# Performance work log

Hardware: AMD Instinct MI355X
Metric: run time of the kernel (lower is better)

The kernel has to match this reference:

```python
import jax, jax.numpy as jnp
import numpy as np
import math

FACTOR = 5


def _prob_attention(queries, keys, values, index_sample):
    # queries/keys/values: [B, H, L, D]; index_sample: [L_Q, sample_k] int
    B, H, L_Q, D = queries.shape
    L_K = keys.shape[2]
    u = min(FACTOR * int(math.ceil(math.log(L_Q))), L_Q)  # n_top queries

    # --- _prob_QK: random-sampled scores, heuristic M, top-u query selection ---
    # gather sampled keys per query position: [B, H, L_Q, sample_k, D]
    K_sample = keys[:, :, index_sample, :]
    Q_K_sample = jnp.einsum('bhqd,bhqkd->bhqk', queries, K_sample)  # [B,H,L_Q,sample_k]
    M = Q_K_sample.max(axis=-1) - Q_K_sample.sum(axis=-1) / L_K      # [B,H,L_Q]
    M_top = jax.lax.top_k(M, u)[1]                                   # [B,H,u] indices

    # gather the selected queries and compute full scores against all keys
    Q_reduce = jnp.take_along_axis(queries, M_top[..., None], axis=2)  # [B,H,u,D]
    scores = jnp.einsum('bhud,bhkd->bhuk', Q_reduce, keys)             # [B,H,u,L_K]

    # scale: original does `scale = self.scale or 1/sqrt(D)`; with scale=True this
    # multiplies by True (i.e. *1), so scores are left unscaled -- faithful.

    # --- causal ProbMask: triu(1) rows gathered at the selected query indices ---
    causal = jnp.triu(jnp.ones((L_Q, L_K), dtype=bool), 1)  # [L_Q, L_K]
    row_mask = causal[M_top]                                 # [B,H,u,L_K]
    scores = jnp.where(row_mask, -jnp.inf, scores)

    attn = jax.nn.softmax(scores, axis=-1)                   # [B,H,u,L_K]

    # --- initial context (mask_flag=True): cumulative sum of V over time ---
    context = jnp.cumsum(values, axis=2)                     # [B,H,L_Q,D]

    # --- scatter-update context at selected query positions ---
    upd = jnp.einsum('bhuk,bhkd->bhud', attn, values)        # [B,H,u,D]
    b_idx = jnp.arange(B)[:, None, None]
    h_idx = jnp.arange(H)[None, :, None]
    context = context.at[b_idx, h_idx, M_top].set(upd)

    return jnp.transpose(context, (0, 2, 1, 3))              # [B,L_Q,H,D]


def setup_inputs() -> dict:
    key = jax.random.key(0)
    kq, kk, kv, ki = jax.random.split(key, 4)
    B, H, L, D = 4, 8, 2048, 64
    sample_k = FACTOR * int(math.ceil(math.log(L)))  # 40
    queries = jax.random.normal(kq, (B, H, L, D), dtype=jnp.float32)
    keys = jax.random.normal(kk, (B, H, L, D), dtype=jnp.float32)
    values = jax.random.normal(kv, (B, H, L, D), dtype=jnp.float32)
    index_sample = jax.random.randint(ki, (L, sample_k), 0, L)
    return {"queries": queries, "keys": keys, "values": values,
            "index_sample": index_sample}


def reference(queries, keys, values, index_sample):
    return _prob_attention(queries, keys, values, index_sample)
```

## Files before the change

kernel.cpp:

```cpp
#include <hip/hip_runtime.h>
#include <math.h>

#define B_ 4
#define H_ 8
#define L_ 2048
#define D_ 64
#define SK_ 40
#define U_ 40
#define CK 256
#define NCHUNK (L_ / CK)
#define QG 8
#define NQG (U_ / QG)
#define CSB 32
#define SEG2 16
#define NSEG2 (L_ / SEG2)
#define PB 256

__global__ __launch_bounds__(1024) void k_mcs(
    const float* __restrict__ Q, const float* __restrict__ K,
    const int* __restrict__ idxs, const float* __restrict__ V,
    float* __restrict__ M, float* __restrict__ pfx) {
  if (blockIdx.x < CSB) {
    __shared__ float wt[16][64];
    int bh = blockIdx.x;
    int w = threadIdx.x >> 6, lane = threadIdx.x & 63;
    const float* Vb = V + (size_t)bh * L_ * D_;
    float pres[8];
    float pre = 0.f;
#pragma unroll
    for (int i = 0; i < 8; ++i) {
      int base = w * 128 + i * SEG2;
      float s = 0.f;
      for (int l = 0; l < SEG2; ++l) s += Vb[(size_t)(base + l) * D_ + lane];
      pres[i] = pre;
      pre += s;
    }
    wt[w][lane] = pre;
    __syncthreads();
    float base = 0.f;
    for (int ww = 0; ww < 16; ++ww) {
      float v = wt[ww][lane];
      if (ww < w) base += v;
    }
#pragma unroll
    for (int i = 0; i < 8; ++i)
      pfx[((size_t)bh * NSEG2 + w * 8 + i) * D_ + lane] = base + pres[i];
    return;
  }

  int blk = blockIdx.x - CSB;
  int x = blk & 7;
  int j = blk >> 3;
  int bh = ((j >> 7) << 3) | x;
  int qc = j & 127;
  int wave = threadIdx.x >> 6;
  int lane = threadIdx.x & 63;
  int q = qc * 16 + wave;

  int g  = lane >> 3;
  int li = lane & 7;

  const float4* qrow = (const float4*)(Q + ((size_t)bh * L_ + q) * D_);
  float4 qa = qrow[li], qb = qrow[li + 8];
  int myidx = (lane < SK_) ? idxs[q * SK_ + lane] : 0;
  const float* Kb = K + (size_t)bh * L_ * D_;

  int kis[5];
#pragma unroll
  for (int t = 0; t < 5; ++t) kis[t] = __shfl(myidx, t * 8 + g, 64);

  float4 ka[5], kb[5];
#pragma unroll
  for (int t = 0; t < 5; ++t) {
    const float4* kr = (const float4*)(Kb + (size_t)kis[t] * D_);
    ka[t] = kr[li];
    kb[t] = kr[li + 8];
  }

  float d[5];
#pragma unroll
  for (int t = 0; t < 5; ++t) {
    d[t] = qa.x * ka[t].x + qa.y * ka[t].y + qa.z * ka[t].z + qa.w * ka[t].w
         + qb.x * kb[t].x + qb.y * kb[t].y + qb.z * kb[t].z + qb.w * kb[t].w;
  }
  float mx = -INFINITY, sm = 0.f;
#pragma unroll
  for (int t = 0; t < 5; ++t) {
    float v = d[t];
    v += __shfl_xor(v, 1, 64);
    v += __shfl_xor(v, 2, 64);
    v += __shfl_xor(v, 4, 64);
    mx = fmaxf(mx, v);
    sm += v;
  }
  mx = fmaxf(mx, __shfl_xor(mx, 8, 64));
  mx = fmaxf(mx, __shfl_xor(mx, 16, 64));
  mx = fmaxf(mx, __shfl_xor(mx, 32, 64));
  sm += __shfl_xor(sm, 8, 64);
  sm += __shfl_xor(sm, 16, 64);
  sm += __shfl_xor(sm, 32, 64);
  if (lane == 0) M[bh * L_ + q] = mx - sm * (1.0f / (float)L_);
}

__global__ __launch_bounds__(1024) void k_topk(
    const float* __restrict__ M, const float* __restrict__ V,
    const float* __restrict__ pfx, int* __restrict__ Mtop,
    float* __restrict__ out) {
  if (blockIdx.x >= CSB) {
    int bid = blockIdx.x - CSB;
    int bh = bid >> 3, oct = bid & 7;
    int b = bh >> 3, h = bh & 7;
    int w = threadIdx.x >> 6, lane = threadIdx.x & 63;
    int seg = oct * 16 + w;
    float run = pfx[((size_t)bh * NSEG2 + seg) * D_ + lane];
    const float* Vb = V + (size_t)bh * L_ * D_;
    int base = seg * SEG2;
    for (int l = 0; l < SEG2; ++l) {
      int gl = base + l;
      run += Vb[(size_t)gl * D_ + lane];
      out[(((size_t)b * L_ + gl) * H_ + h) * D_ + lane] = run;
    }
    return;
  }

  __shared__ unsigned keys[L_];
  __shared__ int hist[256];
  __shared__ int Gs[256];
  __shared__ unsigned ctl_prefix;
  __shared__ int ctl_need, ctl_cnt, ctl_min;
  __shared__ int wmin[16];
  int bh = blockIdx.x;
  int tid = threadIdx.x;

  for (int i = tid; i < L_; i += 1024) {
    unsigned u = __float_as_uint(M[bh * L_ + i]);
    keys[i] = (u & 0x80000000u) ? ~u : (u | 0x80000000u);
  }
  if (tid == 0) { ctl_prefix = 0u; ctl_need = U_; ctl_cnt = 0; }
  __syncthreads();

  unsigned prefix = 0u, pmask = 0u;
#pragma unroll
  for (int pass = 0; pass < 4; ++pass) {
    int shift = 24 - 8 * pass;
    if (tid < 256) hist[tid] = 0;
    __syncthreads();
    for (int i = tid; i < L_; i += 1024) {
      unsigned k = keys[i];
      if ((k & pmask) == prefix) atomicAdd(&hist[(k >> shift) & 0xffu], 1);
    }
    __syncthreads();
    if (tid < 64) {
      int b0 = tid * 4;
      int h0 = hist[b0], h1 = hist[b0 + 1], h2 = hist[b0 + 2], h3 = hist[b0 + 3];
      int gs = h0 + h1 + h2 + h3;
      int S = gs;
#pragma unroll
      for (int d = 1; d < 64; d <<= 1) {
        int v = __shfl_down(S, d, 64);
        if (tid + d < 64) S += v;
      }
      int E = S - gs;
      Gs[b0 + 3] = E;
      Gs[b0 + 2] = E + h3;
      Gs[b0 + 1] = E + h3 + h2;
      Gs[b0 + 0] = E + h3 + h2 + h1;
    }
    __syncthreads();
    int need = ctl_need;
    if (tid < 256) {
      int G = Gs[tid], h = hist[tid];
      if (G < need && need <= G + h) {
        ctl_prefix = prefix | ((unsigned)tid << shift);
        ctl_need = need - G;
      }
    }
    __syncthreads();
    prefix = ctl_prefix;
    pmask |= (0xffu << shift);
  }

  unsigned v40 = prefix;
  int tiesNeeded = ctl_need;
  __syncthreads();

  for (int i = tid; i < L_; i += 1024) {
    if (keys[i] > v40) {
      int slot = atomicAdd(&ctl_cnt, 1);
      Mtop[bh * U_ + slot] = i;
    }
  }
  __syncthreads();
  int base = ctl_cnt;
  int last = -1;
  for (int t = 0; t < tiesNeeded; ++t) {
    int lmin = 0x7fffffff;
    for (int i = tid; i < L_; i += 1024)
      if (keys[i] == v40 && i > last) lmin = min(lmin, i);
#pragma unroll
    for (int d = 32; d > 0; d >>= 1) lmin = min(lmin, __shfl_xor(lmin, d, 64));
    if ((tid & 63) == 0) wmin[tid >> 6] = lmin;
    __syncthreads();
    if (tid == 0) {
      int m = wmin[0];
      for (int w = 1; w < 16; ++w) m = min(m, wmin[w]);
      Mtop[bh * U_ + base + t] = m;
      ctl_min = m;
    }
    __syncthreads();
    last = ctl_min;
  }
}

__global__ __launch_bounds__(256) void k_attn_part(
    const float* __restrict__ Q, const float* __restrict__ K,
    const float* __restrict__ V, const int* __restrict__ Mtop,
    float* __restrict__ pm, float* __restrict__ ps, float* __restrict__ pacc) {
  int blk = blockIdx.x;
  int x = blk & 7;
  int j = blk >> 3;
  int bh = (j / 40) * 8 + x;
  int rem = j % 40;
  int c  = rem / NQG;
  int qg = rem % NQG;

  int tid = threadIdx.x;
  int w = tid >> 6, lane = tid & 63;
  __shared__ float Qs[QG][D_];
  __shared__ float P[QG][CK];
  __shared__ float pvred[4][QG][D_];
  __shared__ int q0s[QG];
  if (tid < QG) q0s[tid] = Mtop[bh * U_ + qg * QG + tid];
  __syncthreads();
  for (int i = tid; i < QG * D_; i += 256) {
    int u = i >> 6, d = i & 63;
    Qs[u][d] = Q[((size_t)bh * L_ + q0s[u]) * D_ + d];
  }
  __syncthreads();

  int kg = c * CK + tid;
  const float4* kr = (const float4*)(K + ((size_t)bh * L_ + kg) * D_);
  float4 kv[16];
#pragma unroll
  for (int j4 = 0; j4 < 16; ++j4) kv[j4] = kr[j4];
#pragma unroll
  for (int u = 0; u < QG; ++u) {
    float acc = 0.f;
#pragma unroll
    for (int j4 = 0; j4 < 16; ++j4) {
      float4 qv = *(const float4*)&Qs[u][j4 * 4];
      acc += qv.x * kv[j4].x + qv.y * kv[j4].y + qv.z * kv[j4].z + qv.w * kv[j4].w;
    }
    P[u][tid] = (kg <= q0s[u]) ? acc : -INFINITY;
  }
  __syncthreads();

#pragma unroll
  for (int uu = 0; uu < 2; ++uu) {
    int u = w * 2 + uu;
    float v0 = P[u][lane], v1 = P[u][lane + 64];
    float v2 = P[u][lane + 128], v3 = P[u][lane + 192];
    float m = fmaxf(fmaxf(v0, v1), fmaxf(v2, v3));
    for (int o = 32; o > 0; o >>= 1) m = fmaxf(m, __shfl_xor(m, o, 64));
    float e0 = (v0 == -INFINITY) ? 0.f : expf(v0 - m);
    float e1 = (v1 == -INFINITY) ? 0.f : expf(v1 - m);
    float e2 = (v2 == -INFINITY) ? 0.f : expf(v2 - m);
    float e3 = (v3 == -INFINITY) ? 0.f : expf(v3 - m);
    float s = e0 + e1 + e2 + e3;
    for (int o = 32; o > 0; o >>= 1) s += __shfl_xor(s, o, 64);
    P[u][lane] = e0; P[u][lane + 64] = e1;
    P[u][lane + 128] = e2; P[u][lane + 192] = e3;
    if (lane == 0) {
      int p = (bh * NCHUNK + c) * U_ + qg * QG + u;
      pm[p] = m; ps[p] = s;
    }
  }
  __syncthreads();

  const float* Vb = V + ((size_t)bh * L_ + c * CK + w * 64) * D_;
  float acc[QG];
#pragma unroll
  for (int u = 0; u < QG; ++u) acc[u] = 0.f;
  for (int k4 = 0; k4 < 16; ++k4) {
    float4 pv[QG];
#pragma unroll
    for (int u = 0; u < QG; ++u) pv[u] = *(const float4*)&P[u][w * 64 + k4 * 4];
    float va = Vb[(size_t)(k4 * 4 + 0) * D_ + lane];
    float vb = Vb[(size_t)(k4 * 4 + 1) * D_ + lane];
    float vc = Vb[(size_t)(k4 * 4 + 2) * D_ + lane];
    float vd = Vb[(size_t)(k4 * 4 + 3) * D_ + lane];
#pragma unroll
    for (int u = 0; u < QG; ++u)
      acc[u] += pv[u].x * va + pv[u].y * vb + pv[u].z * vc + pv[u].w * vd;
  }
#pragma unroll
  for (int u = 0; u < QG; ++u) pvred[w][u][lane] = acc[u];
  __syncthreads();
#pragma unroll
  for (int uu = 0; uu < 2; ++uu) {
    int u = w * 2 + uu;
    float tot = pvred[0][u][lane] + pvred[1][u][lane] +
                pvred[2][u][lane] + pvred[3][u][lane];
    int p = (bh * NCHUNK + c) * U_ + qg * QG + u;
    pacc[(size_t)p * 64 + lane] = tot;
  }
}

__global__ __launch_bounds__(256) void k_attn_reduce(
    const float* __restrict__ pm, const float* __restrict__ ps,
    const float* __restrict__ pacc, const int* __restrict__ Mtop,
    float* __restrict__ out) {
  int g = blockIdx.x * 4 + (threadIdx.x >> 6);
  int lane = threadIdx.x & 63;
  int bh = g / U_, u = g % U_;
  int b = bh >> 3, h = bh & 7;
  int q0 = Mtop[bh * U_ + u];
  float pmv[NCHUNK];
  float M = -INFINITY;
#pragma unroll
  for (int c = 0; c < NCHUNK; ++c) {
    pmv[c] = pm[(bh * NCHUNK + c) * U_ + u];
    M = fmaxf(M, pmv[c]);
  }
  float T = 0.f, o = 0.f;
#pragma unroll
  for (int c = 0; c < NCHUNK; ++c) {
    float wgt = (pmv[c] == -INFINITY) ? 0.f : expf(pmv[c] - M);
    T += ps[(bh * NCHUNK + c) * U_ + u] * wgt;
    o += pacc[((size_t)(bh * NCHUNK + c) * U_ + u) * 64 + lane] * wgt;
  }
  out[(((size_t)b * L_ + q0) * H_ + h) * D_ + lane] = o / T;
}

extern "C" void kernel_launch(void* const* d_in, const int* in_sizes, int n_in,
                              void* d_out, int out_size, void* d_ws, size_t ws_size,
                              hipStream_t stream) {
  const float* Q = (const float*)d_in[0];
  const float* K = (const float*)d_in[1];
  const float* V = (const float*)d_in[2];
  const int* idxs = (const int*)d_in[3];
  float* out = (float*)d_out;

  char* ws = (char*)d_ws;
  float* M    = (float*)(ws + 0);
  float* pfx  = (float*)(ws + 262144);
  int*   Mtop = (int*)(ws + 1310720);
  float* pm   = (float*)(ws + 1318912);
  float* ps   = (float*)(ws + 1359872);
  float* pacc = (float*)(ws + 1400832);

  k_mcs<<<CSB + (B_ * H_ * L_) / 16, 1024, 0, stream>>>(Q, K, idxs, V, M, pfx);
  k_topk<<<CSB + PB, 1024, 0, stream>>>(M, V, pfx, Mtop, out);
  k_attn_part<<<B_ * H_ * NCHUNK * NQG, 256, 0, stream>>>(Q, K, V, Mtop, pm, ps, pacc);
  k_attn_reduce<<<(B_ * H_ * U_) / 4, 256, 0, stream>>>(pm, ps, pacc, Mtop, out);
}
```

Measured before the change: 68.47 us.

## Stage K chunks in shared memory and bucket sampled indices per chunk for M

The sampled-score kernel now loads each head's keys in 512-row chunks into 128KB of swizzled LDS. Each thread handles one query and reads its sampled keys from LDS, using a per-chunk index list that a new setup kernel builds, instead of gathering random K rows from global memory. The V prefix-sum work moves into that setup kernel with a different block shape. This trades random global gathers for a full streaming read of K per query block, adding an extra launch and grid sizes that give few blocks per head (256 total), with divergent inner loops over variable slot counts.

```diff
diff --git a/kernel.cpp b/kernel.cpp
--- a/kernel.cpp
+++ b/kernel.cpp
@@ -15,91 +15,97 @@
 #define SEG2 16
 #define NSEG2 (L_ / SEG2)
 #define PB 256
-
-__global__ __launch_bounds__(1024) void k_mcs(
+#define KCH 4
+#define KROWS 512
+#define SORTB 8
+
+__global__ __launch_bounds__(256) void k_setup(
+    const int* __restrict__ idxs, const float* __restrict__ V,
+    unsigned short* __restrict__ list, float* __restrict__ pfx) {
+  if (blockIdx.x < SORTB) {
+    int q = blockIdx.x * 256 + threadIdx.x;
+    int c0 = 0, c1 = 0, c2 = 0, c3 = 0;
+#pragma unroll
+    for (int s = 0; s < SK_; ++s) {
+      int ki = idxs[q * SK_ + s];
+      int c = ki >> 9;
+      int pos = (c == 0) ? c0 : ((c == 1) ? c1 : ((c == 2) ? c2 : c3));
+      list[(c * SK_ + pos) * L_ + q] = (unsigned short)ki;
+      c0 += (c == 0); c1 += (c == 1); c2 += (c == 2); c3 += (c == 3);
+    }
+#pragma unroll
+    for (int slot = 0; slot < SK_; ++slot) {
+      if (slot >= c0) list[(0 * SK_ + slot) * L_ + q] = 0xFFFFu;
+      if (slot >= c1) list[(1 * SK_ + slot) * L_ + q] = 0xFFFFu;
+      if (slot >= c2) list[(2 * SK_ + slot) * L_ + q] = 0xFFFFu;
+      if (slot >= c3) list[(3 * SK_ + slot) * L_ + q] = 0xFFFFu;
+    }
+    return;
+  }
+  __shared__ float wt[4][64];
+  int bh = blockIdx.x - SORTB;
+  int d = threadIdx.x & 63, grp = threadIdx.x >> 6;
+  const float* Vb = V + (size_t)bh * L_ * D_;
+  float pres[32];
+  float run = 0.f;
+#pragma unroll
+  for (int i = 0; i < 32; ++i) {
+    int base = grp * 512 + i * SEG2;
+    float s = 0.f;
+    for (int l = 0; l < SEG2; ++l) s += Vb[(size_t)(base + l) * D_ + d];
+    pres[i] = run; run += s;
+  }
+  wt[grp][d] = run;
+  __syncthreads();
+  float b0 = 0.f;
+  for (int g = 0; g < 4; ++g) if (g < grp) b0 += wt[g][d];
+#pragma unroll
+  for (int i = 0; i < 32; ++i)
+    pfx[((size_t)bh * NSEG2 + grp * 32 + i) * D_ + d] = b0 + pres[i];
+}
+
+__global__ __launch_bounds__(256) void k_compute_M(
     const float* __restrict__ Q, const float* __restrict__ K,
-    const int* __restrict__ idxs, const float* __restrict__ V,
-    float* __restrict__ M, float* __restrict__ pfx) {
-  if (blockIdx.x < CSB) {
-    __shared__ float wt[16][64];
-    int bh = blockIdx.x;
-    int w = threadIdx.x >> 6, lane = threadIdx.x & 63;
-    const float* Vb = V + (size_t)bh * L_ * D_;
-    float pres[8];
-    float pre = 0.f;
-#pragma unroll
-    for (int i = 0; i < 8; ++i) {
-      int base = w * 128 + i * SEG2;
-      float s = 0.f;
-      for (int l = 0; l < SEG2; ++l) s += Vb[(size_t)(base + l) * D_ + lane];
-      pres[i] = pre;
-      pre += s;
-    }
-    wt[w][lane] = pre;
-    __syncthreads();
-    float base = 0.f;
-    for (int ww = 0; ww < 16; ++ww) {
-      float v = wt[ww][lane];
-      if (ww < w) base += v;
-    }
-#pragma unroll
-    for (int i = 0; i < 8; ++i)
-      pfx[((size_t)bh * NSEG2 + w * 8 + i) * D_ + lane] = base + pres[i];
-    return;
-  }
-
-  int blk = blockIdx.x - CSB;
-  int x = blk & 7;
-  int j = blk >> 3;
-  int bh = ((j >> 7) << 3) | x;
-  int qc = j & 127;
-  int wave = threadIdx.x >> 6;
-  int lane = threadIdx.x & 63;
-  int q = qc * 16 + wave;
-
-  int g  = lane >> 3;
-  int li = lane & 7;
+    const unsigned short* __restrict__ list, float* __restrict__ M) {
+  extern __shared__ float kch[];
+  int x = blockIdx.x & 7;
+  int j = blockIdx.x >> 3;
+  int bh = (j >> 3) * 8 + x;
+  int qblk = j & 7;
+  int tid = threadIdx.x;
+  int q = qblk * 256 + tid;
 
   const float4* qrow = (const float4*)(Q + ((size_t)bh * L_ + q) * D_);
-  float4 qa = qrow[li], qb = qrow[li + 8];
-  int myidx = (lane < SK_) ? idxs[q * SK_ + lane] : 0;
-  const float* Kb = K + (size_t)bh * L_ * D_;
-
-  int kis[5];
-#pragma unroll
-  for (int t = 0; t < 5; ++t) kis[t] = __shfl(myidx, t * 8 + g, 64);
-
-  float4 ka[5], kb[5];
-#pragma unroll
-  for (int t = 0; t < 5; ++t) {
-    const float4* kr = (const float4*)(Kb + (size_t)kis[t] * D_);
-    ka[t] = kr[li];
-    kb[t] = kr[li + 8];
-  }
-
-  float d[5];
-#pragma unroll
-  for (int t = 0; t < 5; ++t) {
-    d[t] = qa.x * ka[t].x + qa.y * ka[t].y + qa.z * ka[t].z + qa.w * ka[t].w
-         + qb.x * kb[t].x + qb.y * kb[t].y + qb.z * kb[t].z + qb.w * kb[t].w;
-  }
+  float4 q4[16];
+#pragma unroll
+  for (int i = 0; i < 16; ++i) q4[i] = qrow[i];
+
   float mx = -INFINITY, sm = 0.f;
-#pragma unroll
-  for (int t = 0; t < 5; ++t) {
-    float v = d[t];
-    v += __shfl_xor(v, 1, 64);
-    v += __shfl_xor(v, 2, 64);
-    v += __shfl_xor(v, 4, 64);
-    mx = fmaxf(mx, v);
-    sm += v;
-  }
-  mx = fmaxf(mx, __shfl_xor(mx, 8, 64));
-  mx = fmaxf(mx, __shfl_xor(mx, 16, 64));
-  mx = fmaxf(mx, __shfl_xor(mx, 32, 64));
-  sm += __shfl_xor(sm, 8, 64);
-  sm += __shfl_xor(sm, 16, 64);
-  sm += __shfl_xor(sm, 32, 64);
-  if (lane == 0) M[bh * L_ + q] = mx - sm * (1.0f / (float)L_);
+  for (int c = 0; c < KCH; ++c) {
+    __syncthreads();
+    const float4* Ks = (const float4*)(K + ((size_t)bh * L_ + c * KROWS) * D_);
+    for (int f = tid; f < KROWS * 16; f += 256) {
+      int r = f >> 4, j4 = f & 15;
+      float4 v = Ks[f];
+      *(float4*)&kch[r * 64 + ((j4 ^ (r & 15)) << 2)] = v;
+    }
+    __syncthreads();
+    for (int slot = 0; slot < SK_; ++slot) {
+      unsigned short e = list[(c * SK_ + slot) * L_ + q];
+      if (__ballot(e != 0xFFFFu) == 0ull) break;
+      int local = e & (KROWS - 1);
+      float a0 = 0.f, a1 = 0.f, a2 = 0.f, a3 = 0.f;
+#pragma unroll
+      for (int j4 = 0; j4 < 16; ++j4) {
+        float4 kv = *(const float4*)&kch[local * 64 + ((j4 ^ (local & 15)) << 2)];
+        a0 += q4[j4].x * kv.x; a1 += q4[j4].y * kv.y;
+        a2 += q4[j4].z * kv.z; a3 += q4[j4].w * kv.w;
+      }
+      float dd = (a0 + a1) + (a2 + a3);
+      if (e != 0xFFFFu) { mx = fmaxf(mx, dd); sm += dd; }
+    }
+  }
+  M[(size_t)bh * L_ + q] = mx - sm * (1.0f / (float)L_);
 }
 
 __global__ __launch_bounds__(1024) void k_topk(
@@ -348,8 +354,13 @@
   float* pm   = (float*)(ws + 1318912);
   float* ps   = (float*)(ws + 1359872);
   float* pacc = (float*)(ws + 1400832);
-
-  k_mcs<<<CSB + (B_ * H_ * L_) / 16, 1024, 0, stream>>>(Q, K, idxs, V, M, pfx);
+  unsigned short* list = (unsigned short*)(ws + 4022272);
+
+  (void)hipFuncSetAttribute((const void*)k_compute_M,
+                            hipFuncAttributeMaxDynamicSharedMemorySize, 131072);
+
+  k_setup<<<SORTB + 32, 256, 0, stream>>>(idxs, V, list, pfx);
+  k_compute_M<<<256, 256, 131072, stream>>>(Q, K, list, M);
   k_topk<<<CSB + PB, 1024, 0, stream>>>(M, V, pfx, Mtop, out);
   k_attn_part<<<B_ * H_ * NCHUNK * NQG, 256, 0, stream>>>(Q, K, V, Mtop, pm, ps, pacc);
   k_attn_reduce<<<(B_ * H_ * U_) / 4, 256, 0, stream>>>(pm, ps, pacc, Mtop, out);
```

After: 175.3 us. +156.1%, slower.

## Fuse attention reduce into partial kernel via last-block atomic counter

Applied to the files above, without the earlier changes.

Drops the separate k_attn_reduce launch. Each (bh, query-group) keeps an atomic counter, zeroed in k_topk, and the last chunk block to finish does the cross-chunk softmax merge and writes the output rows. This saves one kernel launch and its gap, in exchange for threadfences, an atomic per block, and a serial tail of work in the last-arriving blocks.

```diff
diff --git a/kernel.cpp b/kernel.cpp
--- a/kernel.cpp
+++ b/kernel.cpp
@@ -105,7 +105,7 @@
 __global__ __launch_bounds__(1024) void k_topk(
     const float* __restrict__ M, const float* __restrict__ V,
     const float* __restrict__ pfx, int* __restrict__ Mtop,
-    float* __restrict__ out) {
+    float* __restrict__ out, int* __restrict__ cnt) {
   if (blockIdx.x >= CSB) {
     int bid = blockIdx.x - CSB;
     int bh = bid >> 3, oct = bid & 7;
@@ -132,6 +132,8 @@
   int bh = blockIdx.x;
   int tid = threadIdx.x;
 
+  if (tid < NQG) cnt[bh * NQG + tid] = 0;
+
   for (int i = tid; i < L_; i += 1024) {
     unsigned u = __float_as_uint(M[bh * L_ + i]);
     keys[i] = (u & 0x80000000u) ? ~u : (u | 0x80000000u);
@@ -215,7 +217,8 @@
 __global__ __launch_bounds__(256) void k_attn_part(
     const float* __restrict__ Q, const float* __restrict__ K,
     const float* __restrict__ V, const int* __restrict__ Mtop,
-    float* __restrict__ pm, float* __restrict__ ps, float* __restrict__ pacc) {
+    float* __restrict__ pm, float* __restrict__ ps, float* __restrict__ pacc,
+    int* __restrict__ cnt, float* __restrict__ out) {
   int blk = blockIdx.x;
   int x = blk & 7;
   int j = blk >> 3;
@@ -230,6 +233,7 @@
   __shared__ float P[QG][CK];
   __shared__ float pvred[4][QG][D_];
   __shared__ int q0s[QG];
+  __shared__ int isLast;
   if (tid < QG) q0s[tid] = Mtop[bh * U_ + qg * QG + tid];
   __syncthreads();
   for (int i = tid; i < QG * D_; i += 256) {
@@ -304,32 +308,34 @@
     int p = (bh * NCHUNK + c) * U_ + qg * QG + u;
     pacc[(size_t)p * 64 + lane] = tot;
   }
-}
-
-__global__ __launch_bounds__(256) void k_attn_reduce(
-    const float* __restrict__ pm, const float* __restrict__ ps,
-    const float* __restrict__ pacc, const int* __restrict__ Mtop,
-    float* __restrict__ out) {
-  int g = blockIdx.x * 4 + (threadIdx.x >> 6);
-  int lane = threadIdx.x & 63;
-  int bh = g / U_, u = g % U_;
+
+  __threadfence();
+  if (tid == 0)
+    isLast = (atomicAdd(&cnt[bh * NQG + qg], 1) == NCHUNK - 1);
+  __syncthreads();
+  if (!isLast) return;
+  __threadfence();
+
   int b = bh >> 3, h = bh & 7;
-  int q0 = Mtop[bh * U_ + u];
-  float pmv[NCHUNK];
-  float M = -INFINITY;
-#pragma unroll
-  for (int c = 0; c < NCHUNK; ++c) {
-    pmv[c] = pm[(bh * NCHUNK + c) * U_ + u];
-    M = fmaxf(M, pmv[c]);
-  }
-  float T = 0.f, o = 0.f;
-#pragma unroll
-  for (int c = 0; c < NCHUNK; ++c) {
-    float wgt = (pmv[c] == -INFINITY) ? 0.f : expf(pmv[c] - M);
-    T += ps[(bh * NCHUNK + c) * U_ + u] * wgt;
-    o += pacc[((size_t)(bh * NCHUNK + c) * U_ + u) * 64 + lane] * wgt;
-  }
-  out[(((size_t)b * L_ + q0) * H_ + h) * D_ + lane] = o / T;
+#pragma unroll
+  for (int uu = 0; uu < 2; ++uu) {
+    int u = qg * QG + w * 2 + uu;
+    float pmv[NCHUNK];
+    float Mx = -INFINITY;
+#pragma unroll
+    for (int c2 = 0; c2 < NCHUNK; ++c2) {
+      pmv[c2] = pm[(bh * NCHUNK + c2) * U_ + u];
+      Mx = fmaxf(Mx, pmv[c2]);
+    }
+    float T = 0.f, o = 0.f;
+#pragma unroll
+    for (int c2 = 0; c2 < NCHUNK; ++c2) {
+      float wgt = (pmv[c2] == -INFINITY) ? 0.f : expf(pmv[c2] - Mx);
+      T += ps[(bh * NCHUNK + c2) * U_ + u] * wgt;
+      o += pacc[((size_t)(bh * NCHUNK + c2) * U_ + u) * 64 + lane] * wgt;
+    }
+    out[(((size_t)b * L_ + q0s[w * 2 + uu]) * H_ + h) * D_ + lane] = o / T;
+  }
 }
 
 extern "C" void kernel_launch(void* const* d_in, const int* in_sizes, int n_in,
@@ -348,9 +354,10 @@
   float* pm   = (float*)(ws + 1318912);
   float* ps   = (float*)(ws + 1359872);
   float* pacc = (float*)(ws + 1400832);
+  int*   cnt  = (int*)(ws + 4022272);
 
   k_mcs<<<CSB + (B_ * H_ * L_) / 16, 1024, 0, stream>>>(Q, K, idxs, V, M, pfx);
-  k_topk<<<CSB + PB, 1024, 0, stream>>>(M, V, pfx, Mtop, out);
-  k_attn_part<<<B_ * H_ * NCHUNK * NQG, 256, 0, stream>>>(Q, K, V, Mtop, pm, ps, pacc);
-  k_attn_reduce<<<(B_ * H_ * U_) / 4, 256, 0, stream>>>(pm, ps, pacc, Mtop, out);
+  k_topk<<<CSB + PB, 1024, 0, stream>>>(M, V, pfx, Mtop, out, cnt);
+  k_attn_part<<<B_ * H_ * NCHUNK * NQG, 256, 0, stream>>>(
+      Q, K, V, Mtop, pm, ps, pacc, cnt, out);
 }
```

After: 176.6 us. 2.58x slower.
